# Kernel tuning notes

Hardware: AMD Instinct MI355X
Metric: run time of the kernel (lower is better)

Reference implementation:

```python
import jax, jax.numpy as jnp
import numpy as np

N = 100000
E = 1600000
D_IN = 64
D_HID = 64
D_OUT = 64
R = 8
BN_EPS = 1e-5


def setup_inputs() -> dict:
    key = jax.random.key(0)
    ks = jax.random.split(key, 12)
    x = jax.random.normal(ks[0], (N, D_IN), dtype=jnp.float32)
    edge_index = jax.random.randint(ks[1], (2, E), 0, N, dtype=jnp.int64)
    edge_type = jax.random.randint(ks[2], (E,), 0, R, dtype=jnp.int64)
    s1 = 1.0 / np.sqrt(D_IN)
    s2 = 1.0 / np.sqrt(D_HID)
    w1 = jax.random.uniform(ks[3], (R, D_IN, D_HID), jnp.float32, -s1, s1)
    root1 = jax.random.uniform(ks[4], (D_IN, D_HID), jnp.float32, -s1, s1)
    b1 = jnp.zeros((D_HID,), jnp.float32)
    gamma1 = jnp.ones((D_HID,), jnp.float32)
    beta1 = jnp.zeros((D_HID,), jnp.float32)
    w2 = jax.random.uniform(ks[5], (R, D_HID, D_OUT), jnp.float32, -s2, s2)
    root2 = jax.random.uniform(ks[6], (D_HID, D_OUT), jnp.float32, -s2, s2)
    b2 = jnp.zeros((D_OUT,), jnp.float32)
    return {"x": x, "edge_index": edge_index, "edge_type": edge_type,
            "w1": w1, "root1": root1, "b1": b1, "gamma1": gamma1, "beta1": beta1,
            "w2": w2, "root2": root2, "b2": b2}


def rgcn_conv(x, edge_index, edge_type, W, root, bias):
    # PyG RGCNConv with aggr='mean': per relation r, mean of neighbor features
    # over incoming edges of type r, transformed by W[r]; plus root transform + bias.
    # Aggregate-then-transform (legal since transform is linear): one fused
    # segment_sum keyed by (dst, relation), then a grouped GEMM via einsum.
    n, d = x.shape
    src, dst = edge_index[0], edge_index[1]
    seg = dst * R + edge_type                     # [E] combined segment id
    msg = x[src]                                  # [E, d] gather
    agg = jax.ops.segment_sum(msg, seg, num_segments=n * R).reshape(n, R, d)
    cnt = jax.ops.segment_sum(jnp.ones((src.shape[0],), x.dtype), seg,
                              num_segments=n * R).reshape(n, R, 1)
    mean = agg / jnp.maximum(cnt, 1.0)            # [n, R, d]
    return jnp.einsum('nrd,rdo->no', mean, W) + x @ root + bias


def batch_norm(h, gamma, beta):
    mu = h.mean(axis=0)
    var = h.var(axis=0)
    return gamma * (h - mu) * jax.lax.rsqrt(var + BN_EPS) + beta


def reference(x, edge_index, edge_type, w1, root1, b1, gamma1, beta1, w2, root2, b2):
    h = rgcn_conv(x, edge_index, edge_type, w1, root1, b1)
    h = jax.nn.relu(batch_norm(h, gamma1, beta1))
    # dropout: identity (eval mode)
    out = rgcn_conv(h, edge_index, edge_type, w2, root2, b2)
    return out
```

## Files before the change

kernel.cpp:

```cpp
#include <hip/hip_runtime.h>
#include <hip/hip_bf16.h>

#define NN 100000
#define EE 1600000
#define RR 8
#define DD 64
#define MM (NN * RR)
#define BN_EPS 1e-5f
#define KTOT 576

#define NB 391
#define EPB 8192
#define NBIN ((EE + EPB - 1) / EPB)

typedef __bf16 bf16x8 __attribute__((ext_vector_type(8)));
typedef float  f32x4  __attribute__((ext_vector_type(4)));

static __device__ __forceinline__ unsigned short f32_to_bf16(float f) {
    unsigned int u = __float_as_uint(f);
    unsigned int r = u + 0x7FFFu + ((u >> 16) & 1u);
    return (unsigned short)(r >> 16);
}
static __device__ __forceinline__ float bflo(unsigned int u) {
    return __uint_as_float(u << 16);
}
static __device__ __forceinline__ float bfhi(unsigned int u) {
    return __uint_as_float(u & 0xFFFF0000u);
}


__global__ void k_bcount(const int* __restrict__ dst, int* __restrict__ btot) {
    __shared__ int cnt[NB];
    int t = threadIdx.x;
    for (int i = t; i < NB; i += 256) cnt[i] = 0;
    __syncthreads();
    int base = blockIdx.x * EPB;
#pragma unroll
    for (int i = 0; i < EPB / 256; ++i) {
        int e = base + i * 256 + t;
        if (e < EE) atomicAdd(&cnt[dst[e] >> 8], 1);
    }
    __syncthreads();
    for (int i = t; i < NB; i += 256)
        if (cnt[i]) atomicAdd(&btot[i], cnt[i]);
}

__global__ void k_bscan(const int* __restrict__ btot, int* __restrict__ bbase,
                        int* __restrict__ gcur, int* __restrict__ rowptr) {
    __shared__ int sd[512];
    int t = threadIdx.x;
    int v = (t < NB) ? btot[t] : 0;
    sd[t] = v;
    __syncthreads();
    for (int off = 1; off < 512; off <<= 1) {
        int x = (t >= off) ? sd[t - off] : 0;
        __syncthreads();
        sd[t] += x;
        __syncthreads();
    }
    if (t < NB) { bbase[t] = sd[t] - v; gcur[t] = sd[t] - v; }
    if (t == NB - 1) { bbase[NB] = sd[t]; rowptr[MM] = sd[t]; }
}

__global__ void k_bin(const int* __restrict__ src, const int* __restrict__ dst,
                      const int* __restrict__ et, int* __restrict__ gcur,
                      unsigned int* __restrict__ ebuf) {
    __shared__ int cnt[NB];
    __shared__ int bas[NB];
    __shared__ int off[NB];
    int t = threadIdx.x;
    for (int i = t; i < NB; i += 256) { cnt[i] = 0; off[i] = 0; }
    __syncthreads();
    int base = blockIdx.x * EPB;
#pragma unroll
    for (int i = 0; i < EPB / 256; ++i) {
        int e = base + i * 256 + t;
        if (e < EE) atomicAdd(&cnt[dst[e] >> 8], 1);
    }
    __syncthreads();
    for (int i = t; i < NB; i += 256) {
        int c = cnt[i];
        bas[i] = c ? atomicAdd(&gcur[i], c) : 0;
    }
    __syncthreads();
#pragma unroll
    for (int i = 0; i < EPB / 256; ++i) {
        int e = base + i * 256 + t;
        if (e < EE) {
            int d = dst[e];
            int b = d >> 8;
            int lk = ((d & 255) << 3) | et[e];
            unsigned int rec0 = (unsigned int)src[e] | ((unsigned int)lk << 17);
            int p = bas[b] + atomicAdd(&off[b], 1);
            ebuf[p] = rec0;
        }
    }
}

__global__ __launch_bounds__(256) void k_bcsr(const int* __restrict__ bbase,
                                              const unsigned int* __restrict__ ebuf,
                                              int* __restrict__ rowptr,
                                              int* __restrict__ rec) {
    __shared__ int deg[2048];
    __shared__ int part[256];
    int b = blockIdx.x, t = threadIdx.x;
    int e0 = bbase[b], e1 = bbase[b + 1];
    for (int i = t; i < 2048; i += 256) deg[i] = 0;
    __syncthreads();
    for (int e = e0 + t; e < e1; e += 256) atomicAdd(&deg[ebuf[e] >> 17], 1);
    __syncthreads();
    int loc[8];
    int s = 0;
#pragma unroll
    for (int j = 0; j < 8; ++j) { loc[j] = deg[t * 8 + j]; s += loc[j]; }
    part[t] = s;
    __syncthreads();
    for (int off = 1; off < 256; off <<= 1) {
        int x = (t >= off) ? part[t - off] : 0;
        __syncthreads();
        part[t] += x;
        __syncthreads();
    }
    int run = part[t] - s;
    int keyBase = b * 2048;
#pragma unroll
    for (int j = 0; j < 8; ++j) {
        int g = keyBase + t * 8 + j;
        if (g < MM) rowptr[g] = e0 + run;
        deg[t * 8 + j] = run;
        run += loc[j];
    }
    __syncthreads();
    for (int e = e0 + t; e < e1; e += 256) {
        unsigned int v = ebuf[e];
        int lk = v >> 17;
        int pos = e0 + atomicAdd(&deg[lk], 1);
        rec[pos] = (int)(v & 0x1FFFFu);
    }
}


__global__ void k_tobf16(const float* __restrict__ X, unsigned short* __restrict__ Xb) {
    int i = blockIdx.x * 256 + threadIdx.x;
    if (i >= NN * DD / 4) return;
    float4 v = ((const float4*)X)[i];
    ushort4 o;
    o.x = f32_to_bf16(v.x); o.y = f32_to_bf16(v.y);
    o.z = f32_to_bf16(v.z); o.w = f32_to_bf16(v.w);
    ((ushort4*)Xb)[i] = o;
}


__global__ void k_agg(const unsigned short* __restrict__ Xb,
                      const int* __restrict__ rowptr,
                      const int* __restrict__ rec,
                      unsigned short* __restrict__ mean) {
    int wv = threadIdx.x >> 6;
    int lane = threadIdx.x & 63;
    int n = blockIdx.x * 4 + wv;
    if (n >= NN) return;
    int r = lane >> 3;
    int q = lane & 7;
    int e0 = rowptr[n * RR + r];
    int e1 = rowptr[n * RR + r + 1];
    float a0[8] = {0.f, 0.f, 0.f, 0.f, 0.f, 0.f, 0.f, 0.f};
    float a1[8] = {0.f, 0.f, 0.f, 0.f, 0.f, 0.f, 0.f, 0.f};
    int e = e0;
    for (; e + 1 < e1; e += 2) {
        int s0 = rec[e];
        int s1 = rec[e + 1];
        uint4 u0 = *(const uint4*)(Xb + (size_t)s0 * DD + q * 8);
        uint4 u1 = *(const uint4*)(Xb + (size_t)s1 * DD + q * 8);
        a0[0] += bflo(u0.x); a0[1] += bfhi(u0.x);
        a0[2] += bflo(u0.y); a0[3] += bfhi(u0.y);
        a0[4] += bflo(u0.z); a0[5] += bfhi(u0.z);
        a0[6] += bflo(u0.w); a0[7] += bfhi(u0.w);
        a1[0] += bflo(u1.x); a1[1] += bfhi(u1.x);
        a1[2] += bflo(u1.y); a1[3] += bfhi(u1.y);
        a1[4] += bflo(u1.z); a1[5] += bfhi(u1.z);
        a1[6] += bflo(u1.w); a1[7] += bfhi(u1.w);
    }
    if (e < e1) {
        int s0 = rec[e];
        uint4 u0 = *(const uint4*)(Xb + (size_t)s0 * DD + q * 8);
        a0[0] += bflo(u0.x); a0[1] += bfhi(u0.x);
        a0[2] += bflo(u0.y); a0[3] += bfhi(u0.y);
        a0[4] += bflo(u0.z); a0[5] += bfhi(u0.z);
        a0[6] += bflo(u0.w); a0[7] += bfhi(u0.w);
    }
    int cnt = e1 - e0;
    float inv = 1.0f / (float)(cnt > 1 ? cnt : 1);
    uint4 o;
    o.x = (unsigned)f32_to_bf16((a0[0] + a1[0]) * inv) | ((unsigned)f32_to_bf16((a0[1] + a1[1]) * inv) << 16);
    o.y = (unsigned)f32_to_bf16((a0[2] + a1[2]) * inv) | ((unsigned)f32_to_bf16((a0[3] + a1[3]) * inv) << 16);
    o.z = (unsigned)f32_to_bf16((a0[4] + a1[4]) * inv) | ((unsigned)f32_to_bf16((a0[5] + a1[5]) * inv) << 16);
    o.w = (unsigned)f32_to_bf16((a0[6] + a1[6]) * inv) | ((unsigned)f32_to_bf16((a0[7] + a1[7]) * inv) << 16);
    *(uint4*)(mean + (size_t)n * 512 + r * 64 + q * 8) = o;
}


__global__ void k_prepw(const float* __restrict__ W, const float* __restrict__ Root,
                        unsigned short* __restrict__ WcT) {
    int i = blockIdx.x * 256 + threadIdx.x;
    if (i >= 64 * KTOT) return;
    int o = i / KTOT;
    int k = i - o * KTOT;
    float v;
    if (k < 512) v = W[(size_t)(k >> 6) * 4096 + (k & 63) * 64 + o];
    else         v = Root[(k - 512) * 64 + o];
    WcT[(size_t)o * KTOT + k] = f32_to_bf16(v);
}


__global__ __launch_bounds__(256) void k_gemm(const unsigned short* __restrict__ meanB,
                                              const unsigned short* __restrict__ Xb,
                                              const unsigned short* __restrict__ WcT,
                                              const float* __restrict__ bias,
                                              float* __restrict__ Out) {
    int t = threadIdx.x;
    int wv = t >> 6, lane = t & 63;
    int quad = lane >> 4, m16 = lane & 15;
    int row0 = blockIdx.x * 128 + wv * 32;
    int r0 = row0 + m16;
    int r1 = row0 + 16 + m16;
    bool ok0 = r0 < NN, ok1 = r1 < NN;

    union AU { uint4 u; bf16x8 f; };
    f32x4 acc[2][4];
#pragma unroll
    for (int i = 0; i < 2; ++i)
#pragma unroll
        for (int j = 0; j < 4; ++j) acc[i][j] = (f32x4){0.f, 0.f, 0.f, 0.f};

    const unsigned short* a0p = meanB + (size_t)r0 * 512 + quad * 8;
    const unsigned short* a1p = meanB + (size_t)r1 * 512 + quad * 8;
    const unsigned short* x0p = Xb + (size_t)r0 * DD + quad * 8;
    const unsigned short* x1p = Xb + (size_t)r1 * DD + quad * 8;
    const unsigned short* wp  = WcT + (size_t)m16 * KTOT + quad * 8;

#pragma unroll
    for (int kb = 0; kb < 16; ++kb) {
        AU av0, av1, bv[4];
        if (ok0) av0.u = *(const uint4*)(a0p + kb * 32); else av0.u = make_uint4(0,0,0,0);
        if (ok1) av1.u = *(const uint4*)(a1p + kb * 32); else av1.u = make_uint4(0,0,0,0);
#pragma unroll
        for (int nt = 0; nt < 4; ++nt)
            bv[nt].u = *(const uint4*)(wp + (size_t)nt * 16 * KTOT + kb * 32);
#pragma unroll
        for (int nt = 0; nt < 4; ++nt) {
            acc[0][nt] = __builtin_amdgcn_mfma_f32_16x16x32_bf16(av0.f, bv[nt].f, acc[0][nt], 0, 0, 0);
            acc[1][nt] = __builtin_amdgcn_mfma_f32_16x16x32_bf16(av1.f, bv[nt].f, acc[1][nt], 0, 0, 0);
        }
    }
#pragma unroll
    for (int kb = 0; kb < 2; ++kb) {
        AU av0, av1, bv[4];
        if (ok0) av0.u = *(const uint4*)(x0p + kb * 32); else av0.u = make_uint4(0,0,0,0);
        if (ok1) av1.u = *(const uint4*)(x1p + kb * 32); else av1.u = make_uint4(0,0,0,0);
#pragma unroll
        for (int nt = 0; nt < 4; ++nt)
            bv[nt].u = *(const uint4*)(wp + (size_t)nt * 16 * KTOT + 512 + kb * 32);
#pragma unroll
        for (int nt = 0; nt < 4; ++nt) {
            acc[0][nt] = __builtin_amdgcn_mfma_f32_16x16x32_bf16(av0.f, bv[nt].f, acc[0][nt], 0, 0, 0);
            acc[1][nt] = __builtin_amdgcn_mfma_f32_16x16x32_bf16(av1.f, bv[nt].f, acc[1][nt], 0, 0, 0);
        }
    }

#pragma unroll
    for (int rt = 0; rt < 2; ++rt) {
#pragma unroll
        for (int nt = 0; nt < 4; ++nt) {
            int col = nt * 16 + m16;
            float bb = bias[col];
#pragma unroll
            for (int i = 0; i < 4; ++i) {
                int row = row0 + rt * 16 + quad * 4 + i;
                if (row < NN) Out[(size_t)row * 64 + col] = acc[rt][nt][i] + bb;
            }
        }
    }
}


__global__ void k_colstats(const float* __restrict__ H, float* __restrict__ stats) {
    int t = threadIdx.x;
    int col = t & 63;
    int rl = t >> 6;
    float s = 0.f, sq = 0.f;
    for (int n = blockIdx.x * 4 + rl; n < NN; n += gridDim.x * 4) {
        float v = H[(size_t)n * 64 + col];
        s += v;
        sq += v * v;
    }
    __shared__ float ss[256], sv[256];
    ss[t] = s; sv[t] = sq;
    __syncthreads();
    if (t < 128) { ss[t] += ss[t + 128]; sv[t] += sv[t + 128]; }
    __syncthreads();
    if (t < 64) {
        atomicAdd(&stats[col], ss[t] + ss[t + 64]);
        atomicAdd(&stats[64 + col], sv[t] + sv[t + 64]);
    }
}

__global__ void k_bnrelu(float* __restrict__ H, unsigned short* __restrict__ Hb,
                         const float* __restrict__ stats,
                         const float* __restrict__ gamma, const float* __restrict__ beta) {
    int idx = blockIdx.x * 256 + threadIdx.x;
    const int total = NN * DD / 4;
    if (idx >= total) return;
    int c0 = (idx & 15) * 4;
    float4 v = ((const float4*)H)[idx];
    float inv = 1.0f / (float)NN;
    float4 o;
    {
        float mu = stats[c0 + 0] * inv;
        float var = stats[64 + c0 + 0] * inv - mu * mu;
        float sc = gamma[c0 + 0] * rsqrtf(var + BN_EPS);
        float r = sc * (v.x - mu) + beta[c0 + 0];
        o.x = r > 0.f ? r : 0.f;
    }
    {
        float mu = stats[c0 + 1] * inv;
        float var = stats[64 + c0 + 1] * inv - mu * mu;
        float sc = gamma[c0 + 1] * rsqrtf(var + BN_EPS);
        float r = sc * (v.y - mu) + beta[c0 + 1];
        o.y = r > 0.f ? r : 0.f;
    }
    {
        float mu = stats[c0 + 2] * inv;
        float var = stats[64 + c0 + 2] * inv - mu * mu;
        float sc = gamma[c0 + 2] * rsqrtf(var + BN_EPS);
        float r = sc * (v.z - mu) + beta[c0 + 2];
        o.z = r > 0.f ? r : 0.f;
    }
    {
        float mu = stats[c0 + 3] * inv;
        float var = stats[64 + c0 + 3] * inv - mu * mu;
        float sc = gamma[c0 + 3] * rsqrtf(var + BN_EPS);
        float r = sc * (v.w - mu) + beta[c0 + 3];
        o.w = r > 0.f ? r : 0.f;
    }
    ((float4*)H)[idx] = o;
    ushort4 ob;
    ob.x = f32_to_bf16(o.x); ob.y = f32_to_bf16(o.y);
    ob.z = f32_to_bf16(o.z); ob.w = f32_to_bf16(o.w);
    ((ushort4*)Hb)[idx] = ob;
}


static inline size_t alignup(size_t x) { return (x + 255) & ~(size_t)255; }

extern "C" void kernel_launch(void* const* d_in, const int* in_sizes, int n_in,
                              void* d_out, int out_size, void* d_ws, size_t ws_size,
                              hipStream_t stream) {
    const float* x      = (const float*)d_in[0];
    const int*   eidx   = (const int*)d_in[1];
    const int*   etype  = (const int*)d_in[2];
    const float* w1     = (const float*)d_in[3];
    const float* root1  = (const float*)d_in[4];
    const float* b1     = (const float*)d_in[5];
    const float* gamma1 = (const float*)d_in[6];
    const float* beta1  = (const float*)d_in[7];
    const float* w2     = (const float*)d_in[8];
    const float* root2  = (const float*)d_in[9];
    const float* b2     = (const float*)d_in[10];
    float* out = (float*)d_out;

    const int* src = eidx;
    const int* dst = eidx + EE;

    char* w = (char*)d_ws;
    int* rowptr = (int*)w;            w += alignup((size_t)(MM + 1) * 4);
    int* btot   = (int*)w;            w += alignup(512 * 4);
    int* bbase  = (int*)w;            w += alignup(512 * 4);
    int* gcur   = (int*)w;            w += alignup(512 * 4);
    int* rec    = (int*)w;            w += alignup((size_t)EE * 4);
    unsigned short* mean = (unsigned short*)w; w += alignup((size_t)NN * 512 * 2);
    float* h    = (float*)w;          w += alignup((size_t)NN * DD * 4);
    unsigned short* xhb = (unsigned short*)w; w += alignup((size_t)NN * DD * 2);
    unsigned short* wct1 = (unsigned short*)w; w += alignup((size_t)64 * KTOT * 2);
    unsigned short* wct2 = (unsigned short*)w; w += alignup((size_t)64 * KTOT * 2);
    float* stats = (float*)w;         w += alignup(128 * 4);
    unsigned int* ebuf = (unsigned int*)mean;

    hipMemsetAsync(btot, 0, 512 * 4, stream);
    hipMemsetAsync(stats, 0, 128 * 4, stream);

    k_prepw<<<dim3(144), dim3(256), 0, stream>>>(w1, root1, wct1);
    k_prepw<<<dim3(144), dim3(256), 0, stream>>>(w2, root2, wct2);
    k_tobf16<<<dim3(NN * DD / 4 / 256 + 1), dim3(256), 0, stream>>>(x, xhb);

    k_bcount<<<dim3(NBIN), dim3(256), 0, stream>>>(dst, btot);
    k_bscan<<<dim3(1), dim3(512), 0, stream>>>(btot, bbase, gcur, rowptr);
    k_bin<<<dim3(NBIN), dim3(256), 0, stream>>>(src, dst, etype, gcur, ebuf);
    k_bcsr<<<dim3(NB), dim3(256), 0, stream>>>(bbase, ebuf, rowptr, rec);

    k_agg<<<dim3((NN + 3) / 4), dim3(256), 0, stream>>>(xhb, rowptr, rec, mean);
    k_gemm<<<dim3((NN + 127) / 128), dim3(256), 0, stream>>>(mean, xhb, wct1, b1, h);
    k_colstats<<<dim3(256), dim3(256), 0, stream>>>(h, stats);
    k_bnrelu<<<dim3(NN * DD / 4 / 256), dim3(256), 0, stream>>>(h, xhb, stats, gamma1, beta1);

    k_agg<<<dim3((NN + 3) / 4), dim3(256), 0, stream>>>(xhb, rowptr, rec, mean);
    k_gemm<<<dim3((NN + 127) / 128), dim3(256), 0, stream>>>(mean, xhb, wct2, b2, out);
}
```

Before: 422.8 us.

## Fuse BN column stats into GEMM, stage weights in LDS, unroll aggregation by four

The batch-norm column sum and sum-of-squares are now computed in the GEMM epilogue with wave shuffles and shared-memory reduction. This removes the separate k_colstats pass that re-read the hidden activations. The GEMM also stages the combined weight matrix in padded LDS instead of reading it from global memory per wave. The aggregation loop now keeps four gathers in flight instead of two. The cost is about 75KB of LDS per GEMM block, which may lower occupancy, plus extra register pressure in k_agg.

```diff
diff --git a/kernel.cpp b/kernel.cpp
--- a/kernel.cpp
+++ b/kernel.cpp
@@ -8,6 +8,7 @@
 #define MM (NN * RR)
 #define BN_EPS 1e-5f
 #define KTOT 576
+#define BSTRIDE 584
 
 #define NB 391
 #define EPB 8192
@@ -163,38 +164,49 @@
     int q = lane & 7;
     int e0 = rowptr[n * RR + r];
     int e1 = rowptr[n * RR + r + 1];
-    float a0[8] = {0.f, 0.f, 0.f, 0.f, 0.f, 0.f, 0.f, 0.f};
-    float a1[8] = {0.f, 0.f, 0.f, 0.f, 0.f, 0.f, 0.f, 0.f};
+    float a0[8] = {0,0,0,0,0,0,0,0};
+    float a1[8] = {0,0,0,0,0,0,0,0};
+    float a2[8] = {0,0,0,0,0,0,0,0};
+    float a3[8] = {0,0,0,0,0,0,0,0};
     int e = e0;
-    for (; e + 1 < e1; e += 2) {
-        int s0 = rec[e];
-        int s1 = rec[e + 1];
+    for (; e + 3 < e1; e += 4) {
+        int s0 = rec[e], s1 = rec[e + 1], s2 = rec[e + 2], s3 = rec[e + 3];
         uint4 u0 = *(const uint4*)(Xb + (size_t)s0 * DD + q * 8);
         uint4 u1 = *(const uint4*)(Xb + (size_t)s1 * DD + q * 8);
-        a0[0] += bflo(u0.x); a0[1] += bfhi(u0.x);
-        a0[2] += bflo(u0.y); a0[3] += bfhi(u0.y);
-        a0[4] += bflo(u0.z); a0[5] += bfhi(u0.z);
-        a0[6] += bflo(u0.w); a0[7] += bfhi(u0.w);
-        a1[0] += bflo(u1.x); a1[1] += bfhi(u1.x);
-        a1[2] += bflo(u1.y); a1[3] += bfhi(u1.y);
-        a1[4] += bflo(u1.z); a1[5] += bfhi(u1.z);
-        a1[6] += bflo(u1.w); a1[7] += bfhi(u1.w);
+        uint4 u2 = *(const uint4*)(Xb + (size_t)s2 * DD + q * 8);
+        uint4 u3 = *(const uint4*)(Xb + (size_t)s3 * DD + q * 8);
+        a0[0] += bflo(u0.x); a0[1] += bfhi(u0.x); a0[2] += bflo(u0.y); a0[3] += bfhi(u0.y);
+        a0[4] += bflo(u0.z); a0[5] += bfhi(u0.z); a0[6] += bflo(u0.w); a0[7] += bfhi(u0.w);
+        a1[0] += bflo(u1.x); a1[1] += bfhi(u1.x); a1[2] += bflo(u1.y); a1[3] += bfhi(u1.y);
+        a1[4] += bflo(u1.z); a1[5] += bfhi(u1.z); a1[6] += bflo(u1.w); a1[7] += bfhi(u1.w);
+        a2[0] += bflo(u2.x); a2[1] += bfhi(u2.x); a2[2] += bflo(u2.y); a2[3] += bfhi(u2.y);
+        a2[4] += bflo(u2.z); a2[5] += bfhi(u2.z); a2[6] += bflo(u2.w); a2[7] += bfhi(u2.w);
+        a3[0] += bflo(u3.x); a3[1] += bfhi(u3.x); a3[2] += bflo(u3.y); a3[3] += bfhi(u3.y);
+        a3[4] += bflo(u3.z); a3[5] += bfhi(u3.z); a3[6] += bflo(u3.w); a3[7] += bfhi(u3.w);
+    }
+    if (e + 1 < e1) {
+        int s0 = rec[e], s1 = rec[e + 1];
+        uint4 u0 = *(const uint4*)(Xb + (size_t)s0 * DD + q * 8);
+        uint4 u1 = *(const uint4*)(Xb + (size_t)s1 * DD + q * 8);
+        a0[0] += bflo(u0.x); a0[1] += bfhi(u0.x); a0[2] += bflo(u0.y); a0[3] += bfhi(u0.y);
+        a0[4] += bflo(u0.z); a0[5] += bfhi(u0.z); a0[6] += bflo(u0.w); a0[7] += bfhi(u0.w);
+        a1[0] += bflo(u1.x); a1[1] += bfhi(u1.x); a1[2] += bflo(u1.y); a1[3] += bfhi(u1.y);
+        a1[4] += bflo(u1.z); a1[5] += bfhi(u1.z); a1[6] += bflo(u1.w); a1[7] += bfhi(u1.w);
+        e += 2;
     }
     if (e < e1) {
         int s0 = rec[e];
         uint4 u0 = *(const uint4*)(Xb + (size_t)s0 * DD + q * 8);
-        a0[0] += bflo(u0.x); a0[1] += bfhi(u0.x);
-        a0[2] += bflo(u0.y); a0[3] += bfhi(u0.y);
-        a0[4] += bflo(u0.z); a0[5] += bfhi(u0.z);
-        a0[6] += bflo(u0.w); a0[7] += bfhi(u0.w);
+        a0[0] += bflo(u0.x); a0[1] += bfhi(u0.x); a0[2] += bflo(u0.y); a0[3] += bfhi(u0.y);
+        a0[4] += bflo(u0.z); a0[5] += bfhi(u0.z); a0[6] += bflo(u0.w); a0[7] += bfhi(u0.w);
     }
     int cnt = e1 - e0;
     float inv = 1.0f / (float)(cnt > 1 ? cnt : 1);
     uint4 o;
-    o.x = (unsigned)f32_to_bf16((a0[0] + a1[0]) * inv) | ((unsigned)f32_to_bf16((a0[1] + a1[1]) * inv) << 16);
-    o.y = (unsigned)f32_to_bf16((a0[2] + a1[2]) * inv) | ((unsigned)f32_to_bf16((a0[3] + a1[3]) * inv) << 16);
-    o.z = (unsigned)f32_to_bf16((a0[4] + a1[4]) * inv) | ((unsigned)f32_to_bf16((a0[5] + a1[5]) * inv) << 16);
-    o.w = (unsigned)f32_to_bf16((a0[6] + a1[6]) * inv) | ((unsigned)f32_to_bf16((a0[7] + a1[7]) * inv) << 16);
+    o.x = (unsigned)f32_to_bf16((a0[0]+a1[0]+a2[0]+a3[0]) * inv) | ((unsigned)f32_to_bf16((a0[1]+a1[1]+a2[1]+a3[1]) * inv) << 16);
+    o.y = (unsigned)f32_to_bf16((a0[2]+a1[2]+a2[2]+a3[2]) * inv) | ((unsigned)f32_to_bf16((a0[3]+a1[3]+a2[3]+a3[3]) * inv) << 16);
+    o.z = (unsigned)f32_to_bf16((a0[4]+a1[4]+a2[4]+a3[4]) * inv) | ((unsigned)f32_to_bf16((a0[5]+a1[5]+a2[5]+a3[5]) * inv) << 16);
+    o.w = (unsigned)f32_to_bf16((a0[6]+a1[6]+a2[6]+a3[6]) * inv) | ((unsigned)f32_to_bf16((a0[7]+a1[7]+a2[7]+a3[7]) * inv) << 16);
     *(uint4*)(mean + (size_t)n * 512 + r * 64 + q * 8) = o;
 }
 
@@ -216,8 +228,23 @@
                                               const unsigned short* __restrict__ Xb,
                                               const unsigned short* __restrict__ WcT,
                                               const float* __restrict__ bias,
-                                              float* __restrict__ Out) {
+                                              float* __restrict__ Out,
+                                              float* __restrict__ stats,
+                                              int dostats) {
+    __shared__ unsigned short Bs[64 * BSTRIDE];
+    __shared__ float ssum[4][64];
+    __shared__ float ssq[4][64];
     int t = threadIdx.x;
+#pragma unroll
+    for (int i = 0; i < 18; ++i) {
+        int idx = i * 256 + t;
+        int row = idx / 72;
+        int k16 = idx - row * 72;
+        uint4 v = *(const uint4*)(WcT + (size_t)row * KTOT + k16 * 8);
+        *(uint4*)(Bs + row * BSTRIDE + k16 * 8) = v;
+    }
+    __syncthreads();
+
     int wv = t >> 6, lane = t & 63;
     int quad = lane >> 4, m16 = lane & 15;
     int row0 = blockIdx.x * 128 + wv * 32;
@@ -236,7 +263,7 @@
     const unsigned short* a1p = meanB + (size_t)r1 * 512 + quad * 8;
     const unsigned short* x0p = Xb + (size_t)r0 * DD + quad * 8;
     const unsigned short* x1p = Xb + (size_t)r1 * DD + quad * 8;
-    const unsigned short* wp  = WcT + (size_t)m16 * KTOT + quad * 8;
+    const unsigned short* bs  = Bs + m16 * BSTRIDE + quad * 8;
 
 #pragma unroll
     for (int kb = 0; kb < 16; ++kb) {
@@ -245,7 +272,7 @@
         if (ok1) av1.u = *(const uint4*)(a1p + kb * 32); else av1.u = make_uint4(0,0,0,0);
 #pragma unroll
         for (int nt = 0; nt < 4; ++nt)
-            bv[nt].u = *(const uint4*)(wp + (size_t)nt * 16 * KTOT + kb * 32);
+            bv[nt].u = *(const uint4*)(bs + nt * 16 * BSTRIDE + kb * 32);
 #pragma unroll
         for (int nt = 0; nt < 4; ++nt) {
             acc[0][nt] = __builtin_amdgcn_mfma_f32_16x16x32_bf16(av0.f, bv[nt].f, acc[0][nt], 0, 0, 0);
@@ -259,7 +286,7 @@
         if (ok1) av1.u = *(const uint4*)(x1p + kb * 32); else av1.u = make_uint4(0,0,0,0);
 #pragma unroll
         for (int nt = 0; nt < 4; ++nt)
-            bv[nt].u = *(const uint4*)(wp + (size_t)nt * 16 * KTOT + 512 + kb * 32);
+            bv[nt].u = *(const uint4*)(bs + nt * 16 * BSTRIDE + 512 + kb * 32);
 #pragma unroll
         for (int nt = 0; nt < 4; ++nt) {
             acc[0][nt] = __builtin_amdgcn_mfma_f32_16x16x32_bf16(av0.f, bv[nt].f, acc[0][nt], 0, 0, 0);
@@ -280,29 +307,42 @@
             }
         }
     }
-}
-
-
-__global__ void k_colstats(const float* __restrict__ H, float* __restrict__ stats) {
-    int t = threadIdx.x;
-    int col = t & 63;
-    int rl = t >> 6;
-    float s = 0.f, sq = 0.f;
-    for (int n = blockIdx.x * 4 + rl; n < NN; n += gridDim.x * 4) {
-        float v = H[(size_t)n * 64 + col];
-        s += v;
-        sq += v * v;
-    }
-    __shared__ float ss[256], sv[256];
-    ss[t] = s; sv[t] = sq;
-    __syncthreads();
-    if (t < 128) { ss[t] += ss[t + 128]; sv[t] += sv[t + 128]; }
-    __syncthreads();
-    if (t < 64) {
-        atomicAdd(&stats[col], ss[t] + ss[t + 64]);
-        atomicAdd(&stats[64 + col], sv[t] + sv[t + 64]);
-    }
-}
+
+    if (dostats) {
+#pragma unroll
+        for (int nt = 0; nt < 4; ++nt) {
+            int col = nt * 16 + m16;
+            float bb = bias[col];
+            float s = 0.f, sq = 0.f;
+#pragma unroll
+            for (int rt = 0; rt < 2; ++rt) {
+#pragma unroll
+                for (int i = 0; i < 4; ++i) {
+                    int row = row0 + rt * 16 + quad * 4 + i;
+                    if (row < NN) {
+                        float v = acc[rt][nt][i] + bb;
+                        s += v; sq += v * v;
+                    }
+                }
+            }
+            s += __shfl_xor(s, 16); s += __shfl_xor(s, 32);
+            sq += __shfl_xor(sq, 16); sq += __shfl_xor(sq, 32);
+            if (quad == 0) { ssum[wv][col] = s; ssq[wv][col] = sq; }
+        }
+        __syncthreads();
+        if (t < 128) {
+            int col = t & 63;
+            if (t < 64) {
+                float s = ssum[0][col] + ssum[1][col] + ssum[2][col] + ssum[3][col];
+                atomicAdd(&stats[col], s);
+            } else {
+                float sq = ssq[0][col] + ssq[1][col] + ssq[2][col] + ssq[3][col];
+                atomicAdd(&stats[64 + col], sq);
+            }
+        }
+    }
+}
+
 
 __global__ void k_bnrelu(float* __restrict__ H, unsigned short* __restrict__ Hb,
                          const float* __restrict__ stats,
@@ -398,10 +438,9 @@
     k_bcsr<<<dim3(NB), dim3(256), 0, stream>>>(bbase, ebuf, rowptr, rec);
 
     k_agg<<<dim3((NN + 3) / 4), dim3(256), 0, stream>>>(xhb, rowptr, rec, mean);
-    k_gemm<<<dim3((NN + 127) / 128), dim3(256), 0, stream>>>(mean, xhb, wct1, b1, h);
-    k_colstats<<<dim3(256), dim3(256), 0, stream>>>(h, stats);
+    k_gemm<<<dim3((NN + 127) / 128), dim3(256), 0, stream>>>(mean, xhb, wct1, b1, h, stats, 1);
     k_bnrelu<<<dim3(NN * DD / 4 / 256), dim3(256), 0, stream>>>(h, xhb, stats, gamma1, beta1);
 
     k_agg<<<dim3((NN + 3) / 4), dim3(256), 0, stream>>>(xhb, rowptr, rec, mean);
-    k_gemm<<<dim3((NN + 127) / 128), dim3(256), 0, stream>>>(mean, xhb, wct2, b2, out);
-}
+    k_gemm<<<dim3((NN + 127) / 128), dim3(256), 0, stream>>>(mean, xhb, wct2, b2, out, stats, 0);
+}
```

Result: faster. 377.4 us (-10.7%).
